# Kernel tuning notes

Measured on AMD Instinct MI355X. Metric: run time of the kernel, lower is better.

Reference implementation:

```python
import jax, jax.numpy as jnp
import numpy as np
from math import sqrt

NUM_HEADS = 8
N_ELEMENTS = 500_000
D = 256          # input_representation_size
HID = 256        # hidden_size
D_OUT = 256      # output_representation_size
NUM_SAMPLES = 16384


def setup_inputs() -> dict:
    key = jax.random.key(0)
    k1, k2, k3, k4, k5, k6 = jax.random.split(key, 6)
    scale = 1.0 / sqrt(D)
    return {
        "element_embeddings": jax.random.normal(k1, (N_ELEMENTS, D), dtype=jnp.float32),
        "element_to_sample_map": jnp.sort(
            jax.random.randint(k2, (N_ELEMENTS,), 0, NUM_SAMPLES, dtype=jnp.int32)
        ),
        "num_samples": NUM_SAMPLES,
        "Wq": jax.random.normal(k3, (D, HID), dtype=jnp.float32) * scale,
        "Wk": jax.random.normal(k4, (D, HID), dtype=jnp.float32) * scale,
        "Wv": jax.random.normal(k5, (D, HID), dtype=jnp.float32) * scale,
        "Wo": jax.random.normal(k6, (HID, D_OUT), dtype=jnp.float32) * (1.0 / sqrt(HID)),
    }


def reference(element_embeddings, element_to_sample_map, num_samples, Wq, Wk, Wv, Wo):
    N = element_embeddings.shape[0]
    seg = element_to_sample_map
    head_dim = HID // NUM_HEADS

    # --- query summarizer: segment-mean pool then bias-free linear -> [S, HID]
    counts = jax.ops.segment_sum(
        jnp.ones((N,), dtype=element_embeddings.dtype), seg, num_segments=num_samples
    )
    pooled = jax.ops.segment_sum(element_embeddings, seg, num_segments=num_samples)
    pooled = pooled / jnp.maximum(counts, 1.0)[:, None]
    queries = pooled @ Wq                                   # [S, HID]

    # --- per-element queries / keys, split into heads
    q_el = queries[seg].reshape(N, NUM_HEADS, head_dim)     # gather per element
    keys = (element_embeddings @ Wk).reshape(N, NUM_HEADS, head_dim)

    # --- per-head scores + segment log-softmax (stable)
    scores = jnp.einsum("nhd,nhd->nh", q_el, keys) / sqrt(head_dim)  # [N, H]
    seg_max = jax.ops.segment_max(scores, seg, num_segments=num_samples)  # [S, H]
    shifted = scores - seg_max[seg]
    denom = jax.ops.segment_sum(jnp.exp(shifted), seg, num_segments=num_samples)
    probs = jnp.exp(shifted - jnp.log(denom)[seg])          # [N, H]

    # --- value branch, weighted scatter-sum pooling
    values = (element_embeddings @ Wv).reshape(N, NUM_HEADS, head_dim)
    weighted = (probs[..., None] * values).reshape(N, HID)
    per_sample = jax.ops.segment_sum(weighted, seg, num_segments=num_samples)  # [S, HID]

    return per_sample @ Wo
```

## Files before the change

### kernel.cpp

```cpp
#include <hip/hip_runtime.h>
#include <math.h>

#define NELEM 500000
#define NSAMP 16384
#define DIM   256
#define NH    8
#define HDIM  32

__global__ void k0_bounds(const int* __restrict__ seg, int* __restrict__ bounds) {
    int i = blockIdx.x * blockDim.x + threadIdx.x;
    if (i > NSAMP) return;
    int lo = 0, hi = NELEM;
    while (lo < hi) {
        int mid = (lo + hi) >> 1;
        if (seg[mid] < i) lo = mid + 1; else hi = mid;
    }
    bounds[i] = lo;
}

__global__ __launch_bounds__(256) void k1_pool(const float* __restrict__ E,
                                               const int* __restrict__ bounds,
                                               float* __restrict__ pooled) {
    int l = threadIdx.x & 63;
    int s = blockIdx.x * 4 + (threadIdx.x >> 6);
    int start = bounds[s], end = bounds[s + 1];
    const float4* Ev = (const float4*)E;
    float4 a0 = make_float4(0.f, 0.f, 0.f, 0.f);
    float4 a1 = make_float4(0.f, 0.f, 0.f, 0.f);
    float4 a2 = make_float4(0.f, 0.f, 0.f, 0.f);
    float4 a3 = make_float4(0.f, 0.f, 0.f, 0.f);
    int e = start;
    for (; e + 3 < end; e += 4) {
        float4 v0 = Ev[(size_t)(e + 0) * 64 + l];
        float4 v1 = Ev[(size_t)(e + 1) * 64 + l];
        float4 v2 = Ev[(size_t)(e + 2) * 64 + l];
        float4 v3 = Ev[(size_t)(e + 3) * 64 + l];
        a0.x += v0.x; a0.y += v0.y; a0.z += v0.z; a0.w += v0.w;
        a1.x += v1.x; a1.y += v1.y; a1.z += v1.z; a1.w += v1.w;
        a2.x += v2.x; a2.y += v2.y; a2.z += v2.z; a2.w += v2.w;
        a3.x += v3.x; a3.y += v3.y; a3.z += v3.z; a3.w += v3.w;
    }
    for (; e < end; ++e) {
        float4 v0 = Ev[(size_t)e * 64 + l];
        a0.x += v0.x; a0.y += v0.y; a0.z += v0.z; a0.w += v0.w;
    }
    int cnt = end - start;
    float inv = 1.0f / (float)(cnt > 0 ? cnt : 1);
    float4 o;
    o.x = (a0.x + a1.x + a2.x + a3.x) * inv;
    o.y = (a0.y + a1.y + a2.y + a3.y) * inv;
    o.z = (a0.z + a1.z + a2.z + a3.z) * inv;
    o.w = (a0.w + a1.w + a2.w + a3.w) * inv;
    ((float4*)pooled)[(size_t)s * 64 + l] = o;
}

__global__ __launch_bounds__(256) void gemm_256(const float* __restrict__ A,
                                                const float* __restrict__ B,
                                                float* __restrict__ C) {
    __shared__ float As[16][68];
    __shared__ float Bs[16][68];
    int tx = threadIdx.x;
    int m0 = blockIdx.x * 64, n0 = blockIdx.y * 64;
    int ml = (tx >> 4) * 4, nl = (tx & 15) * 4;
    int lam = tx >> 2, lak = (tx & 3) * 4;
    int lbk = tx >> 4, lbn = (tx & 15) * 4;
    float acc[4][4] = {};
    for (int k0 = 0; k0 < 256; k0 += 16) {
        float4 av = *(const float4*)&A[(size_t)(m0 + lam) * 256 + k0 + lak];
        float4 bv = *(const float4*)&B[(size_t)(k0 + lbk) * 256 + n0 + lbn];
        __syncthreads();
        As[lak + 0][lam] = av.x; As[lak + 1][lam] = av.y;
        As[lak + 2][lam] = av.z; As[lak + 3][lam] = av.w;
        *(float4*)&Bs[lbk][lbn] = bv;
        __syncthreads();
#pragma unroll
        for (int k = 0; k < 16; ++k) {
            float4 a4 = *(const float4*)&As[k][ml];
            float4 b4 = *(const float4*)&Bs[k][nl];
            float aa[4] = {a4.x, a4.y, a4.z, a4.w};
            float bb[4] = {b4.x, b4.y, b4.z, b4.w};
#pragma unroll
            for (int i = 0; i < 4; ++i)
#pragma unroll
                for (int j = 0; j < 4; ++j)
                    acc[i][j] = fmaf(aa[i], bb[j], acc[i][j]);
        }
    }
#pragma unroll
    for (int i = 0; i < 4; ++i) {
        float4 o = make_float4(acc[i][0], acc[i][1], acc[i][2], acc[i][3]);
        *(float4*)&C[(size_t)(m0 + ml + i) * 256 + n0 + nl] = o;
    }
}

__global__ __launch_bounds__(256) void k2b_t(const float* __restrict__ q,
                                             const float* __restrict__ Wk,
                                             float* __restrict__ t) {
    __shared__ float wkT[32][256];
    __shared__ float qT[32][64];
    int tx = threadIdx.x;
    int s0 = blockIdx.x * 64, h = blockIdx.y;
#pragma unroll
    for (int it = 0; it < 8; ++it) {
        int idx = tx + it * 256;
        int i = idx >> 3, dq = (idx & 7) * 4;
        float4 v = *(const float4*)&Wk[(size_t)i * 256 + h * 32 + dq];
        wkT[dq + 0][i] = v.x; wkT[dq + 1][i] = v.y;
        wkT[dq + 2][i] = v.z; wkT[dq + 3][i] = v.w;
    }
#pragma unroll
    for (int it = 0; it < 2; ++it) {
        int idx = tx + it * 256;
        int ss = idx >> 3, dq = (idx & 7) * 4;
        float4 v = *(const float4*)&q[(size_t)(s0 + ss) * 256 + h * 32 + dq];
        qT[dq + 0][ss] = v.x; qT[dq + 1][ss] = v.y;
        qT[dq + 2][ss] = v.z; qT[dq + 3][ss] = v.w;
    }
    __syncthreads();
    int sl = (tx >> 4) * 4, i0 = (tx & 15) * 16;
    float acc[4][16] = {};
#pragma unroll 8
    for (int k = 0; k < 32; ++k) {
        float4 q4 = *(const float4*)&qT[k][sl];
        float4 w0 = *(const float4*)&wkT[k][i0];
        float4 w1 = *(const float4*)&wkT[k][i0 + 4];
        float4 w2 = *(const float4*)&wkT[k][i0 + 8];
        float4 w3 = *(const float4*)&wkT[k][i0 + 12];
        float qa[4] = {q4.x, q4.y, q4.z, q4.w};
        float wb[16] = {w0.x, w0.y, w0.z, w0.w, w1.x, w1.y, w1.z, w1.w,
                        w2.x, w2.y, w2.z, w2.w, w3.x, w3.y, w3.z, w3.w};
#pragma unroll
        for (int a = 0; a < 4; ++a)
#pragma unroll
            for (int b = 0; b < 16; ++b)
                acc[a][b] = fmaf(qa[a], wb[b], acc[a][b]);
    }
    const float scale = 0.17677669529663687f;
#pragma unroll
    for (int a = 0; a < 4; ++a)
#pragma unroll
        for (int bq = 0; bq < 4; ++bq) {
            float4 o = make_float4(acc[a][bq * 4 + 0] * scale, acc[a][bq * 4 + 1] * scale,
                                   acc[a][bq * 4 + 2] * scale, acc[a][bq * 4 + 3] * scale);
            *(float4*)&t[(size_t)(s0 + sl + a) * 2048 + h * 256 + i0 + bq * 4] = o;
        }
}

__device__ __forceinline__ void stage_row(const float* __restrict__ E, int e,
                                          float* lds_base, int l) {
    const float* g = E + (size_t)e * 256 + l * 4;
    __builtin_amdgcn_global_load_lds(
        (const __attribute__((address_space(1))) void*)g,
        (__attribute__((address_space(3))) void*)lds_base, 16, 0, 0);
}

__global__ __launch_bounds__(256) void k3_flash(const float* __restrict__ E,
                                                const float* __restrict__ t,
                                                const int* __restrict__ bounds,
                                                float* __restrict__ pw) {
    __shared__ float rows[4][8][256];
    int l = threadIdx.x & 63;
    int w = threadIdx.x >> 6;
    int s = blockIdx.x * 4 + w;
    int start = bounds[s], end = bounds[s + 1];
    int g = l & 7, h = l >> 3;

    float* o_row = pw + (size_t)s * 2048 + h * 256;
    if (start >= end) {
        float4 z = make_float4(0.f, 0.f, 0.f, 0.f);
#pragma unroll
        for (int j = 0; j < 8; ++j) ((float4*)o_row)[g * 8 + j] = z;
        return;
    }

    int idx[8];
#pragma unroll
    for (int j = 0; j < 8; ++j) idx[j] = g * 8 + ((j + g) & 7);

    const float4* t_row = (const float4*)(t + (size_t)s * 2048 + h * 256);
    float4 tv[8];
#pragma unroll
    for (int j = 0; j < 8; ++j) tv[j] = t_row[idx[j]];

    int lim = (end - start < 7) ? end : start + 7;
    for (int e = start; e < lim; ++e)
        stage_row(E, e, &rows[w][e & 7][0], l);

    float m = 0.f, d = 0.f;
    float4 acc[8];
#pragma unroll
    for (int j = 0; j < 8; ++j) acc[j] = make_float4(0.f, 0.f, 0.f, 0.f);

    auto consume = [&](int slot) {
        const float4* rp = (const float4*)&rows[w][slot][0];
        float4 r[8];
#pragma unroll
        for (int j = 0; j < 8; ++j) r[j] = rp[idx[j]];
        float q0 = 0.f, q1 = 0.f, q2 = 0.f, q3 = 0.f;
#pragma unroll
        for (int j = 0; j < 8; j += 4) {
            q0 = fmaf(r[j].x, tv[j].x, q0);
            q0 = fmaf(r[j].y, tv[j].y, q0);
            q0 = fmaf(r[j].z, tv[j].z, q0);
            q0 = fmaf(r[j].w, tv[j].w, q0);
            q1 = fmaf(r[j + 1].x, tv[j + 1].x, q1);
            q1 = fmaf(r[j + 1].y, tv[j + 1].y, q1);
            q1 = fmaf(r[j + 1].z, tv[j + 1].z, q1);
            q1 = fmaf(r[j + 1].w, tv[j + 1].w, q1);
            q2 = fmaf(r[j + 2].x, tv[j + 2].x, q2);
            q2 = fmaf(r[j + 2].y, tv[j + 2].y, q2);
            q2 = fmaf(r[j + 2].z, tv[j + 2].z, q2);
            q2 = fmaf(r[j + 2].w, tv[j + 2].w, q2);
            q3 = fmaf(r[j + 3].x, tv[j + 3].x, q3);
            q3 = fmaf(r[j + 3].y, tv[j + 3].y, q3);
            q3 = fmaf(r[j + 3].z, tv[j + 3].z, q3);
            q3 = fmaf(r[j + 3].w, tv[j + 3].w, q3);
        }
        float sc = (q0 + q1) + (q2 + q3);
        sc += __shfl_xor(sc, 1, 64);
        sc += __shfl_xor(sc, 2, 64);
        sc += __shfl_xor(sc, 4, 64);
        if (sc - m > 20.f) {
            float rs = __expf(m - sc);
            d *= rs;
#pragma unroll
            for (int j = 0; j < 8; ++j) {
                acc[j].x *= rs; acc[j].y *= rs; acc[j].z *= rs; acc[j].w *= rs;
            }
            m = sc;
        }
        float p = __expf(sc - m);
        d += p;
#pragma unroll
        for (int j = 0; j < 8; ++j) {
            acc[j].x = fmaf(p, r[j].x, acc[j].x);
            acc[j].y = fmaf(p, r[j].y, acc[j].y);
            acc[j].z = fmaf(p, r[j].z, acc[j].z);
            acc[j].w = fmaf(p, r[j].w, acc[j].w);
        }
    };

    int e = start;
    for (; e + 7 < end; ++e) {
        asm volatile("s_waitcnt vmcnt(6)" ::: "memory");
        consume(e & 7);
        stage_row(E, e + 7, &rows[w][(e + 7) & 7][0], l);
    }
    asm volatile("s_waitcnt vmcnt(0)" ::: "memory");
    for (; e < end; ++e) consume(e & 7);

    float rd = 1.0f / d;
#pragma unroll
    for (int j = 0; j < 8; ++j) {
        float4 v = make_float4(acc[j].x * rd, acc[j].y * rd, acc[j].z * rd, acc[j].w * rd);
        ((float4*)o_row)[idx[j]] = v;
    }
}

__global__ __launch_bounds__(256) void k4a_ps(const float* __restrict__ pw,
                                              const float* __restrict__ Wv,
                                              float* __restrict__ ps) {
    __shared__ float at[32][68];
    __shared__ float bt[32][36];
    int tx = threadIdx.x;
    int s0 = blockIdx.x * 64, h = blockIdx.y;
    int dd = tx & 31, sl = (tx >> 5) * 8;
    float acc[8] = {};
    for (int k0 = 0; k0 < 256; k0 += 32) {
        __syncthreads();
#pragma unroll
        for (int it = 0; it < 2; ++it) {
            int idx = tx + it * 256;
            int ss = idx >> 3, kq = (idx & 7) * 4;
            float4 v = *(const float4*)&pw[(size_t)(s0 + ss) * 2048 + h * 256 + k0 + kq];
            at[kq + 0][ss] = v.x; at[kq + 1][ss] = v.y;
            at[kq + 2][ss] = v.z; at[kq + 3][ss] = v.w;
        }
        {
            int k = tx >> 3, dq = (tx & 7) * 4;
            float4 v = *(const float4*)&Wv[(size_t)(k0 + k) * 256 + h * 32 + dq];
            *(float4*)&bt[k][dq] = v;
        }
        __syncthreads();
#pragma unroll
        for (int k = 0; k < 32; ++k) {
            float b = bt[k][dd];
            float4 a0 = *(const float4*)&at[k][sl];
            float4 a1 = *(const float4*)&at[k][sl + 4];
            acc[0] = fmaf(a0.x, b, acc[0]); acc[1] = fmaf(a0.y, b, acc[1]);
            acc[2] = fmaf(a0.z, b, acc[2]); acc[3] = fmaf(a0.w, b, acc[3]);
            acc[4] = fmaf(a1.x, b, acc[4]); acc[5] = fmaf(a1.y, b, acc[5]);
            acc[6] = fmaf(a1.z, b, acc[6]); acc[7] = fmaf(a1.w, b, acc[7]);
        }
    }
#pragma unroll
    for (int j = 0; j < 8; ++j)
        ps[(size_t)(s0 + sl + j) * 256 + h * 32 + dd] = acc[j];
}

extern "C" void kernel_launch(void* const* d_in, const int* in_sizes, int n_in,
                              void* d_out, int out_size, void* d_ws, size_t ws_size,
                              hipStream_t stream) {
    const float* E  = (const float*)d_in[0];
    const int* seg  = (const int*)d_in[1];
    const float* Wq = (const float*)d_in[3];
    const float* Wk = (const float*)d_in[4];
    const float* Wv = (const float*)d_in[5];
    const float* Wo = (const float*)d_in[6];
    float* out = (float*)d_out;
    float* ws = (float*)d_ws;

    float* pooled = ws;
    float* q      = ws + 4194304;
    float* t      = ws + 8388608;
    float* pw     = ws + 41943040;
    int* bounds   = (int*)(ws + 75497472);
    float* ps     = pooled;

    k0_bounds<<<(NSAMP + 256) / 256, 256, 0, stream>>>(seg, bounds);
    k1_pool<<<NSAMP / 4, 256, 0, stream>>>(E, bounds, pooled);
    gemm_256<<<dim3(NSAMP / 64, 4), 256, 0, stream>>>(pooled, Wq, q);
    k2b_t<<<dim3(NSAMP / 64, NH), 256, 0, stream>>>(q, Wk, t);
    k3_flash<<<NSAMP / 4, 256, 0, stream>>>(E, t, bounds, pw);
    k4a_ps<<<dim3(NSAMP / 64, NH), 256, 0, stream>>>(pw, Wv, ps);
    gemm_256<<<dim3(NSAMP / 64, 4), 256, 0, stream>>>(ps, Wo, out);
}
```

Baseline: 1.095 ms.

## Split each segment across two wavefronts in pooling and flash kernels

Both the mean-pool and the flash-attention-style kernels now assign two wavefronts per sample, each handling half the segment's rows, then merge the partial results through LDS. The flash kernel merges the halves with online-softmax max/denominator rescaling. The pool kernel also switches to async global-to-LDS staging with a 7-deep pipeline. The aim is to shorten the serial per-wave dependency chain for segments averaging about 30 rows and to raise memory-level parallelism. The cost is twice as many blocks, an extra block barrier, and half the waves idling during the final merge.

```diff
diff --git a/kernel.cpp b/kernel.cpp
--- a/kernel.cpp
+++ b/kernel.cpp
@@ -18,40 +18,56 @@
     bounds[i] = lo;
 }
 
+__device__ __forceinline__ void stage_row(const float* __restrict__ E, int e,
+                                          float* lds_base, int l) {
+    const float* g = E + (size_t)e * 256 + l * 4;
+    __builtin_amdgcn_global_load_lds(
+        (const __attribute__((address_space(1))) void*)g,
+        (__attribute__((address_space(3))) void*)lds_base, 16, 0, 0);
+}
+
 __global__ __launch_bounds__(256) void k1_pool(const float* __restrict__ E,
                                                const int* __restrict__ bounds,
                                                float* __restrict__ pooled) {
+    __shared__ float rows[4][8][256];
     int l = threadIdx.x & 63;
-    int s = blockIdx.x * 4 + (threadIdx.x >> 6);
+    int w = threadIdx.x >> 6;
+    int pair = w >> 1, half = w & 1;
+    int s = blockIdx.x * 2 + pair;
     int start = bounds[s], end = bounds[s + 1];
-    const float4* Ev = (const float4*)E;
-    float4 a0 = make_float4(0.f, 0.f, 0.f, 0.f);
-    float4 a1 = make_float4(0.f, 0.f, 0.f, 0.f);
-    float4 a2 = make_float4(0.f, 0.f, 0.f, 0.f);
-    float4 a3 = make_float4(0.f, 0.f, 0.f, 0.f);
-    int e = start;
-    for (; e + 3 < end; e += 4) {
-        float4 v0 = Ev[(size_t)(e + 0) * 64 + l];
-        float4 v1 = Ev[(size_t)(e + 1) * 64 + l];
-        float4 v2 = Ev[(size_t)(e + 2) * 64 + l];
-        float4 v3 = Ev[(size_t)(e + 3) * 64 + l];
-        a0.x += v0.x; a0.y += v0.y; a0.z += v0.z; a0.w += v0.w;
-        a1.x += v1.x; a1.y += v1.y; a1.z += v1.z; a1.w += v1.w;
-        a2.x += v2.x; a2.y += v2.y; a2.z += v2.z; a2.w += v2.w;
-        a3.x += v3.x; a3.y += v3.y; a3.z += v3.z; a3.w += v3.w;
-    }
-    for (; e < end; ++e) {
-        float4 v0 = Ev[(size_t)e * 64 + l];
-        a0.x += v0.x; a0.y += v0.y; a0.z += v0.z; a0.w += v0.w;
-    }
-    int cnt = end - start;
-    float inv = 1.0f / (float)(cnt > 0 ? cnt : 1);
-    float4 o;
-    o.x = (a0.x + a1.x + a2.x + a3.x) * inv;
-    o.y = (a0.y + a1.y + a2.y + a3.y) * inv;
-    o.z = (a0.z + a1.z + a2.z + a3.z) * inv;
-    o.w = (a0.w + a1.w + a2.w + a3.w) * inv;
-    ((float4*)pooled)[(size_t)s * 64 + l] = o;
+    int n = end - start;
+    int nA = (n + 1) >> 1;
+    int b0 = start + (half ? nA : 0);
+    int b1 = half ? end : start + nA;
+
+    int lim = (b1 - b0 < 7) ? b1 : b0 + 7;
+    for (int e = b0; e < lim; ++e) stage_row(E, e, &rows[w][(e - b0) & 7][0], l);
+
+    float4 acc = make_float4(0.f, 0.f, 0.f, 0.f);
+    int e = b0;
+    for (; e + 7 < b1; ++e) {
+        asm volatile("s_waitcnt vmcnt(6)" ::: "memory");
+        float4 v = *(const float4*)&rows[w][(e - b0) & 7][l * 4];
+        acc.x += v.x; acc.y += v.y; acc.z += v.z; acc.w += v.w;
+        stage_row(E, e + 7, &rows[w][(e + 7 - b0) & 7][0], l);
+    }
+    asm volatile("s_waitcnt vmcnt(0)" ::: "memory");
+    for (; e < b1; ++e) {
+        float4 v = *(const float4*)&rows[w][(e - b0) & 7][l * 4];
+        acc.x += v.x; acc.y += v.y; acc.z += v.z; acc.w += v.w;
+    }
+    if (half == 1) *(float4*)&rows[w][0][l * 4] = acc;
+    __syncthreads();
+    if (half == 0) {
+        float4 p = *(const float4*)&rows[w + 1][0][l * 4];
+        float inv = 1.0f / (float)(n > 0 ? n : 1);
+        float4 o;
+        o.x = (acc.x + p.x) * inv;
+        o.y = (acc.y + p.y) * inv;
+        o.z = (acc.z + p.z) * inv;
+        o.w = (acc.w + p.w) * inv;
+        *(float4*)&pooled[(size_t)s * 256 + l * 4] = o;
+    }
 }
 
 __global__ __launch_bounds__(256) void gemm_256(const float* __restrict__ A,
@@ -146,32 +162,22 @@
         }
 }
 
-__device__ __forceinline__ void stage_row(const float* __restrict__ E, int e,
-                                          float* lds_base, int l) {
-    const float* g = E + (size_t)e * 256 + l * 4;
-    __builtin_amdgcn_global_load_lds(
-        (const __attribute__((address_space(1))) void*)g,
-        (__attribute__((address_space(3))) void*)lds_base, 16, 0, 0);
-}
-
 __global__ __launch_bounds__(256) void k3_flash(const float* __restrict__ E,
                                                 const float* __restrict__ t,
                                                 const int* __restrict__ bounds,
                                                 float* __restrict__ pw) {
     __shared__ float rows[4][8][256];
+    __shared__ float md[2][2][8];
     int l = threadIdx.x & 63;
     int w = threadIdx.x >> 6;
-    int s = blockIdx.x * 4 + w;
+    int pair = w >> 1, half = w & 1;
+    int s = blockIdx.x * 2 + pair;
     int start = bounds[s], end = bounds[s + 1];
+    int n = end - start;
     int g = l & 7, h = l >> 3;
-
-    float* o_row = pw + (size_t)s * 2048 + h * 256;
-    if (start >= end) {
-        float4 z = make_float4(0.f, 0.f, 0.f, 0.f);
-#pragma unroll
-        for (int j = 0; j < 8; ++j) ((float4*)o_row)[g * 8 + j] = z;
-        return;
-    }
+    int nA = (n + 1) >> 1;
+    int b0 = start + (half ? nA : 0);
+    int b1 = half ? end : start + nA;
 
     int idx[8];
 #pragma unroll
@@ -182,9 +188,8 @@
 #pragma unroll
     for (int j = 0; j < 8; ++j) tv[j] = t_row[idx[j]];
 
-    int lim = (end - start < 7) ? end : start + 7;
-    for (int e = start; e < lim; ++e)
-        stage_row(E, e, &rows[w][e & 7][0], l);
+    int lim = (b1 - b0 < 7) ? b1 : b0 + 7;
+    for (int e = b0; e < lim; ++e) stage_row(E, e, &rows[w][(e - b0) & 7][0], l);
 
     float m = 0.f, d = 0.f;
     float4 acc[8];
@@ -240,20 +245,45 @@
         }
     };
 
-    int e = start;
-    for (; e + 7 < end; ++e) {
+    int e = b0;
+    for (; e + 7 < b1; ++e) {
         asm volatile("s_waitcnt vmcnt(6)" ::: "memory");
-        consume(e & 7);
-        stage_row(E, e + 7, &rows[w][(e + 7) & 7][0], l);
+        consume((e - b0) & 7);
+        stage_row(E, e + 7, &rows[w][(e + 7 - b0) & 7][0], l);
     }
     asm volatile("s_waitcnt vmcnt(0)" ::: "memory");
-    for (; e < end; ++e) consume(e & 7);
-
-    float rd = 1.0f / d;
-#pragma unroll
-    for (int j = 0; j < 8; ++j) {
-        float4 v = make_float4(acc[j].x * rd, acc[j].y * rd, acc[j].z * rd, acc[j].w * rd);
-        ((float4*)o_row)[idx[j]] = v;
+    for (; e < b1; ++e) consume((e - b0) & 7);
+
+    if (half == 1) {
+        float4* dump = (float4*)&rows[w][0][0];
+#pragma unroll
+        for (int j = 0; j < 8; ++j) dump[j * 64 + l] = acc[j];
+        if (g == 0) { md[pair][0][h] = m; md[pair][1][h] = d; }
+    }
+    __syncthreads();
+    if (half == 0) {
+        float* o_row = pw + (size_t)s * 2048 + h * 256;
+        if (n == 0) {
+            float4 z = make_float4(0.f, 0.f, 0.f, 0.f);
+#pragma unroll
+            for (int j = 0; j < 8; ++j) ((float4*)o_row)[j] = z;
+        } else {
+            float m1 = md[pair][0][h], d1 = md[pair][1][h];
+            float mstar = fmaxf(m, m1);
+            float a0 = __expf(m - mstar), a1 = __expf(m1 - mstar);
+            float rd = 1.0f / (a0 * d + a1 * d1);
+            const float4* dump = (const float4*)&rows[w + 1][0][0];
+#pragma unroll
+            for (int j = 0; j < 8; ++j) {
+                float4 p = dump[j * 64 + l];
+                float4 v;
+                v.x = (a0 * acc[j].x + a1 * p.x) * rd;
+                v.y = (a0 * acc[j].y + a1 * p.y) * rd;
+                v.z = (a0 * acc[j].z + a1 * p.z) * rd;
+                v.w = (a0 * acc[j].w + a1 * p.w) * rd;
+                ((float4*)o_row)[idx[j]] = v;
+            }
+        }
     }
 }
 
@@ -318,10 +348,10 @@
     float* ps     = pooled;
 
     k0_bounds<<<(NSAMP + 256) / 256, 256, 0, stream>>>(seg, bounds);
-    k1_pool<<<NSAMP / 4, 256, 0, stream>>>(E, bounds, pooled);
+    k1_pool<<<NSAMP / 2, 256, 0, stream>>>(E, bounds, pooled);
     gemm_256<<<dim3(NSAMP / 64, 4), 256, 0, stream>>>(pooled, Wq, q);
     k2b_t<<<dim3(NSAMP / 64, NH), 256, 0, stream>>>(q, Wk, t);
-    k3_flash<<<NSAMP / 4, 256, 0, stream>>>(E, t, bounds, pw);
+    k3_flash<<<NSAMP / 2, 256, 0, stream>>>(E, t, bounds, pw);
     k4a_ps<<<dim3(NSAMP / 64, NH), 256, 0, stream>>>(pw, Wv, ps);
     gemm_256<<<dim3(NSAMP / 64, 4), 256, 0, stream>>>(ps, Wo, out);
 }
```

Result: faster. 1.059 ms (-3.3%).
